# Kernel optimization log

Hardware: AMD Instinct MI355X
Metric: run time of the kernel (lower is better)

Reference implementation:

```python
import jax, jax.numpy as jnp
import numpy as np

B, S, H = 16, 512, 2048
NH, NKV = 16, 4
HD = H // NH  # 128


def _rope_tables(seq_len, dim, dtype):
    inv_freq = 1.0 / (10000.0 ** (jnp.arange(0, dim, 2, dtype=jnp.float32) / dim))
    t = jnp.arange(seq_len, dtype=jnp.float32)
    freqs = jnp.einsum('i,j->ij', t, inv_freq)          # [S, HD/2]
    emb = jnp.concatenate([freqs, freqs], axis=-1)       # [S, HD]
    cos = jnp.cos(emb)[None, None].astype(dtype)         # [1,1,S,HD]
    sin = jnp.sin(emb)[None, None].astype(dtype)
    return cos, sin


def _rotate_half(x):
    x1, x2 = jnp.split(x, 2, axis=-1)
    return jnp.concatenate([-x2, x1], axis=-1)


def setup_inputs() -> dict:
    key = jax.random.key(0)
    kx, kq, kk, kv, ko = jax.random.split(key, 5)
    x = jax.random.normal(kx, (B, S, H), dtype=jnp.float32)
    s = 0.02
    Wq = jax.random.normal(kq, (H, H), dtype=jnp.float32) * s
    Wk = jax.random.normal(kk, (NKV * HD, H), dtype=jnp.float32) * s
    Wv = jax.random.normal(kv, (NKV * HD, H), dtype=jnp.float32) * s
    Wo = jax.random.normal(ko, (H, H), dtype=jnp.float32) * s
    return {"x": x, "Wq": Wq, "Wk": Wk, "Wv": Wv, "Wo": Wo}


def reference(x, Wq, Wk, Wv, Wo):
    b, s, _ = x.shape
    scaling = HD ** -0.5
    # projections (torch Linear: y = x @ W.T, W is [out,in])
    q = jnp.einsum('bsh,oh->bso', x, Wq).reshape(b, s, NH, HD).transpose(0, 2, 1, 3)
    k = jnp.einsum('bsh,oh->bso', x, Wk).reshape(b, s, NKV, HD).transpose(0, 2, 1, 3)
    v = jnp.einsum('bsh,oh->bso', x, Wv).reshape(b, s, NKV, HD).transpose(0, 2, 1, 3)
    cos, sin = _rope_tables(s, HD, x.dtype)
    q = q * cos + _rotate_half(q) * sin
    k = k * cos + _rotate_half(k) * sin
    rep = NH // NKV
    k = jnp.repeat(k, rep, axis=1)  # [b, NH, s, HD]
    v = jnp.repeat(v, rep, axis=1)
    scores = jnp.einsum('bhqd,bhkd->bhqk', q, k) * scaling
    attn = jax.nn.softmax(scores, axis=-1)
    out = jnp.einsum('bhqk,bhkd->bhqd', attn, v)
    out = out.transpose(0, 2, 1, 3).reshape(b, s, H)
    return jnp.einsum('bsh,oh->bso', out, Wo)
```

## Files before the change

### kernel.cpp

```cpp
#include <hip/hip_runtime.h>
#include <stdint.h>


typedef _Float16 f16;
typedef _Float16 f16x4 __attribute__((ext_vector_type(4)));
typedef _Float16 f16x8 __attribute__((ext_vector_type(8)));
typedef float f32x4 __attribute__((ext_vector_type(4)));

#define B_   16
#define S_   512
#define H_   2048
#define NH_  16
#define NKV_ 4
#define HD_  128
#define ATT_SCALE 0.08838834764831843f
#define LOG2_10000_DIV64 0.20762050593045952f

#define AS1 __attribute__((address_space(1)))
#define AS3 __attribute__((address_space(3)))

__device__ __forceinline__ void async16(const void* g, const void* l) {
  __builtin_amdgcn_global_load_lds((const AS1 unsigned int*)(uintptr_t)g,
                                   (AS3 unsigned int*)(uintptr_t)l, 16, 0, 0);
}

__global__ __launch_bounds__(256) void cast_all(const float* __restrict__ x,
                                                const float* __restrict__ wq,
                                                const float* __restrict__ wk,
                                                const float* __restrict__ wv,
                                                const float* __restrict__ wo,
                                                f16* __restrict__ x_h,
                                                f16* __restrict__ w_h,
                                                f16* __restrict__ wo_h) {
  const int i = blockIdx.x * 256 + threadIdx.x;
  const float4* src;
  f16x4* dst;
  if (i < 4194304) {
    src = (const float4*)x + i;            dst = (f16x4*)x_h + i;
  } else if (i < 5242880) {
    int j = i - 4194304;
    src = (const float4*)wq + j;           dst = (f16x4*)w_h + j;
  } else if (i < 5505024) {
    int j = i - 5242880;
    src = (const float4*)wk + j;           dst = (f16x4*)w_h + 1048576 + j;
  } else if (i < 5767168) {
    int j = i - 5505024;
    src = (const float4*)wv + j;           dst = (f16x4*)w_h + 1310720 + j;
  } else {
    int j = i - 5767168;
    src = (const float4*)wo + j;           dst = (f16x4*)wo_h + j;
  }
  float4 v = *src;
  f16x4 o = {(f16)v.x, (f16)v.y, (f16)v.z, (f16)v.w};
  *dst = o;
}

template<int MODE>
__global__ __launch_bounds__(512, 2) void gemm_k(const f16* __restrict__ A,
                                                 const f16* __restrict__ W,
                                                 f16* __restrict__ qo,
                                                 f16* __restrict__ ko,
                                                 f16* __restrict__ vto,
                                                 float* __restrict__ fout) {
  __shared__ __align__(16) f16 As[3][256 * 64];
  __shared__ __align__(16) f16 Bs[3][128 * 64];
  const int K = 2048;
  const int NT = 32;
  const int m0 = blockIdx.x * 256;
  const int n0 = blockIdx.y * 128;
  const int tid = threadIdx.x;
  const int wave = tid >> 6, lane = tid & 63;
  const int quad = lane >> 4, l15 = lane & 15;
  const int wm = wave >> 1, wn = wave & 1;

  const f16* aptr[4];
  const f16* bptr[2];
#pragma unroll
  for (int i = 0; i < 4; ++i) {
    const int L = i * 512 + wave * 64 + lane;
    const int r = L >> 3, s = L & 7;
    aptr[i] = A + (size_t)(m0 + r) * K + (s ^ (r & 7)) * 8;
  }
#pragma unroll
  for (int i = 0; i < 2; ++i) {
    const int L = i * 512 + wave * 64 + lane;
    const int r = L >> 3, s = L & 7;
    bptr[i] = W + (size_t)(n0 + r) * K + (s ^ (r & 7)) * 8;
  }
  const int ldsw = wave * 1024;

  f32x4 acc[4][4] = {};
  f16x8 aC[4], bC[4], aN[4], bN[4];

  auto ldA = [&](f16x8* d, const f16* base, int ks) {
#pragma unroll
    for (int mi = 0; mi < 4; ++mi) {
      const int row = wm * 64 + mi * 16 + l15;
      const int slot = (ks * 4 + quad) ^ (l15 & 7);
      d[mi] = *reinterpret_cast<const f16x8*>(base + row * 64 + slot * 8);
    }
  };
  auto ldB = [&](f16x8* d, const f16* base, int ks) {
#pragma unroll
    for (int ni = 0; ni < 4; ++ni) {
      const int col = wn * 32 + (ni >> 1) * 64 + (ni & 1) * 16 + l15;
      const int slot = (ks * 4 + quad) ^ (l15 & 7);
      d[ni] = *reinterpret_cast<const f16x8*>(base + col * 64 + slot * 8);
    }
  };
  auto mfma16 = [&](const f16x8* Af, const f16x8* Bf) {
#pragma unroll
    for (int mi = 0; mi < 4; ++mi)
#pragma unroll
      for (int ni = 0; ni < 4; ++ni)
        acc[mi][ni] = __builtin_amdgcn_mfma_f32_16x16x32_f16(Af[mi], Bf[ni], acc[mi][ni], 0, 0, 0);
  };

#pragma unroll
  for (int t = 0; t < 2; ++t) {
#pragma unroll
    for (int i = 0; i < 4; ++i)
      async16(aptr[i] + t * 64, (const char*)&As[t][0] + i * 8192 + ldsw);
#pragma unroll
    for (int i = 0; i < 2; ++i)
      async16(bptr[i] + t * 64, (const char*)&Bs[t][0] + i * 8192 + ldsw);
  }
  asm volatile("s_waitcnt vmcnt(6)" ::: "memory");
  __builtin_amdgcn_s_barrier();
  ldA(aC, &As[0][0], 0);
  ldB(bC, &Bs[0][0], 0);

  for (int t = 0; t < NT; ++t) {
    const int buf = t % 3, bufn = (t + 1) % 3, bufs = (t + 2) % 3;
    const int sk = (t + 2) * 64;

    ldA(aN, &As[buf][0], 1);
    ldB(bN, &Bs[buf][0], 1);
    if (t + 2 < NT) {
      async16(aptr[0] + sk, (const char*)&As[bufs][0] + 0 * 8192 + ldsw);
      async16(aptr[1] + sk, (const char*)&As[bufs][0] + 1 * 8192 + ldsw);
      async16(bptr[0] + sk, (const char*)&Bs[bufs][0] + 0 * 8192 + ldsw);
    }
    asm volatile("s_waitcnt lgkmcnt(8)" ::: "memory");
    __builtin_amdgcn_sched_barrier(0);
    __builtin_amdgcn_s_setprio(1);
    mfma16(aC, bC);
    __builtin_amdgcn_s_setprio(0);

    if (t + 1 < NT) {
      if (t + 2 < NT) asm volatile("s_waitcnt vmcnt(3)" ::: "memory");
      else            asm volatile("s_waitcnt vmcnt(0)" ::: "memory");
      __builtin_amdgcn_s_barrier();
    }

    if (t + 1 < NT) {
      ldA(aC, &As[bufn][0], 0);
      ldB(bC, &Bs[bufn][0], 0);
    }
    if (t + 2 < NT) {
      async16(aptr[2] + sk, (const char*)&As[bufs][0] + 2 * 8192 + ldsw);
      async16(aptr[3] + sk, (const char*)&As[bufs][0] + 3 * 8192 + ldsw);
      async16(bptr[1] + sk, (const char*)&Bs[bufs][0] + 1 * 8192 + ldsw);
    }
    if (t + 1 < NT) asm volatile("s_waitcnt lgkmcnt(8)" ::: "memory");
    else            asm volatile("s_waitcnt lgkmcnt(0)" ::: "memory");
    __builtin_amdgcn_sched_barrier(0);
    __builtin_amdgcn_s_setprio(1);
    mfma16(aN, bN);
    __builtin_amdgcn_s_setprio(0);
    if (t + 1 < NT) __builtin_amdgcn_s_barrier();
  }

  if constexpr (MODE == 1) {
    const int b_ = m0 >> 9;
    if (n0 >= 2560) {
      const int h = (n0 - 2560) >> 7;
      f16* vb = vto + ((size_t)b_ * NKV_ + h) * HD_ * S_;
#pragma unroll
      for (int mi = 0; mi < 4; ++mi)
#pragma unroll
        for (int r = 0; r < 4; ++r) {
          const int s = (m0 + wm * 64 + mi * 16 + quad * 4 + r) & 511;
#pragma unroll
          for (int ni = 0; ni < 4; ++ni) {
            const int d = (ni >> 1) * 64 + wn * 32 + (ni & 1) * 16 + l15;
            vb[(size_t)d * S_ + s] = (f16)acc[mi][ni][r];
          }
        }
    } else {
      f16* ob = (n0 < 2048)
          ? (qo + ((size_t)b_ * NH_ + (n0 >> 7)) * S_ * HD_)
          : (ko + ((size_t)b_ * NKV_ + ((n0 - 2048) >> 7)) * S_ * HD_);
      float invf[2];
#pragma unroll
      for (int ni = 0; ni < 2; ++ni)
        invf[ni] = exp2f((float)(wn * 32 + ni * 16 + l15) * -LOG2_10000_DIV64);
#pragma unroll
      for (int mi = 0; mi < 4; ++mi)
#pragma unroll
        for (int r = 0; r < 4; ++r) {
          const int s = (m0 + wm * 64 + mi * 16 + quad * 4 + r) & 511;
          const size_t rb = (size_t)s * HD_;
#pragma unroll
          for (int ni = 0; ni < 2; ++ni) {
            const int d = wn * 32 + ni * 16 + l15;
            float sn, cs;
            __sincosf((float)s * invf[ni], &sn, &cs);
            const float x1 = acc[mi][ni][r], x2 = acc[mi][ni + 2][r];
            ob[rb + d] = (f16)(x1 * cs - x2 * sn);
            ob[rb + d + 64] = (f16)(x2 * cs + x1 * sn);
          }
        }
    }
  } else {
#pragma unroll
    for (int mi = 0; mi < 4; ++mi)
#pragma unroll
      for (int ni = 0; ni < 4; ++ni) {
        const int ncol = n0 + wn * 32 + (ni >> 1) * 64 + (ni & 1) * 16 + l15;
#pragma unroll
        for (int r = 0; r < 4; ++r) {
          const int mrow = m0 + wm * 64 + mi * 16 + quad * 4 + r;
          fout[(size_t)mrow * 2048 + ncol] = acc[mi][ni][r];
        }
      }
  }
}

__global__ __launch_bounds__(512) void attn_kernel(const f16* __restrict__ q,
                                                   const f16* __restrict__ k,
                                                   const f16* __restrict__ vt,
                                                   f16* __restrict__ out) {
  __shared__ __align__(16) f16 Kb[2][64 * 128];
  __shared__ __align__(16) f16 Vb[128 * 64];
  __shared__ __align__(16) f16 Ps[8][32 * 64];

  const int qt = blockIdx.x, h = blockIdx.y, b = blockIdx.z;
  const int kvh = h >> 2;
  const int tid = threadIdx.x;
  const int wave = tid >> 6, lane = tid & 63;
  const int quad = lane >> 4, l15 = lane & 15;

  const f16* qbase = q + (((size_t)b * NH_ + h) * S_ + qt * 256) * HD_;
  const f16* kbase = k + ((size_t)b * NKV_ + kvh) * S_ * HD_;
  const f16* vbase = vt + ((size_t)b * NKV_ + kvh) * HD_ * S_;

  auto stageK = [&](int j) {
    f16* dst = &Kb[j & 1][0];
#pragma unroll
    for (int i = 0; i < 2; ++i) {
      const int L0 = i * 512 + wave * 64;
      const int L = L0 + lane;
      const int r = L >> 4, c = L & 15;
      async16(kbase + (size_t)(j * 64 + r) * HD_ + (c ^ (r & 15)) * 8,
              (const char*)dst + (size_t)L0 * 16);
    }
  };
  auto stageV = [&](int j) {
#pragma unroll
    for (int i = 0; i < 2; ++i) {
      const int L0 = i * 512 + wave * 64;
      const int L = L0 + lane;
      const int r = L >> 3, c = L & 7;
      async16(vbase + (size_t)r * S_ + j * 64 + (c ^ (r & 7)) * 8,
              (const char*)&Vb[0] + (size_t)L0 * 16);
    }
  };

  f16x8 aq[2][4];
#pragma unroll
  for (int mi = 0; mi < 2; ++mi)
#pragma unroll
    for (int ks = 0; ks < 4; ++ks)
      aq[mi][ks] = *reinterpret_cast<const f16x8*>(
          qbase + (size_t)(wave * 32 + mi * 16 + l15) * HD_ + ks * 32 + quad * 8);

  stageK(0);

  f32x4 O[2][8] = {};
  float mrun[2][4], lrun[2][4];
#pragma unroll
  for (int mi = 0; mi < 2; ++mi)
#pragma unroll
    for (int r = 0; r < 4; ++r) { mrun[mi][r] = -3.0e38f; lrun[mi][r] = 0.f; }

  for (int j = 0; j < 8; ++j) {
    asm volatile("s_waitcnt vmcnt(0)" ::: "memory");
    __builtin_amdgcn_s_barrier();
    stageV(j);

    f32x4 Sc[2][4] = {};
#pragma unroll
    for (int ks = 0; ks < 4; ++ks) {
      f16x8 bk[4];
#pragma unroll
      for (int ni = 0; ni < 4; ++ni) {
        const int row = ni * 16 + l15;
        bk[ni] = *reinterpret_cast<const f16x8*>(
            &Kb[j & 1][row * 128 + (((ks * 4 + quad) ^ l15) & 15) * 8]);
      }
#pragma unroll
      for (int mi = 0; mi < 2; ++mi)
#pragma unroll
        for (int ni = 0; ni < 4; ++ni)
          Sc[mi][ni] = __builtin_amdgcn_mfma_f32_16x16x32_f16(aq[mi][ks], bk[ni], Sc[mi][ni], 0, 0, 0);
    }

#pragma unroll
    for (int mi = 0; mi < 2; ++mi)
#pragma unroll
      for (int r = 0; r < 4; ++r) {
        float mx = fmaxf(fmaxf(Sc[mi][0][r], Sc[mi][1][r]),
                         fmaxf(Sc[mi][2][r], Sc[mi][3][r]));
        mx *= ATT_SCALE;
#pragma unroll
        for (int off = 1; off < 16; off <<= 1) mx = fmaxf(mx, __shfl_xor(mx, off));
        const float mnew = fmaxf(mrun[mi][r], mx);
        const float alpha = __expf(mrun[mi][r] - mnew);
        float rs = 0.f;
#pragma unroll
        for (int ni = 0; ni < 4; ++ni) {
          const float pv = __expf(Sc[mi][ni][r] * ATT_SCALE - mnew);
          Sc[mi][ni][r] = pv;
          rs += pv;
        }
#pragma unroll
        for (int off = 1; off < 16; off <<= 1) rs += __shfl_xor(rs, off);
        lrun[mi][r] = lrun[mi][r] * alpha + rs;
        mrun[mi][r] = mnew;
#pragma unroll
        for (int ni = 0; ni < 8; ++ni) O[mi][ni][r] *= alpha;
        const int rowl = mi * 16 + quad * 4 + r;
#pragma unroll
        for (int ni = 0; ni < 4; ++ni) {
          const int col = ni * 16 + l15;
          Ps[wave][rowl * 64 + (((ni * 2 + (l15 >> 3)) ^ (rowl & 7)) << 3) + (l15 & 7)] =
              (f16)Sc[mi][ni][r];
        }
      }

    asm volatile("s_waitcnt vmcnt(0)" ::: "memory");
    __builtin_amdgcn_s_barrier();
    if (j < 7) stageK(j + 1);

#pragma unroll
    for (int ks = 0; ks < 2; ++ks) {
      f16x8 ap[2];
#pragma unroll
      for (int mi = 0; mi < 2; ++mi) {
        const int rowl = mi * 16 + l15;
        ap[mi] = *reinterpret_cast<const f16x8*>(
            &Ps[wave][rowl * 64 + (((ks * 4 + quad) ^ (l15 & 7)) << 3)]);
      }
#pragma unroll
      for (int ni = 0; ni < 8; ++ni) {
        const int row = ni * 16 + l15;
        const f16x8 bv = *reinterpret_cast<const f16x8*>(
            &Vb[row * 64 + (((ks * 4 + quad) ^ (l15 & 7)) << 3)]);
#pragma unroll
        for (int mi = 0; mi < 2; ++mi)
          O[mi][ni] = __builtin_amdgcn_mfma_f32_16x16x32_f16(ap[mi], bv, O[mi][ni], 0, 0, 0);
      }
    }
  }

#pragma unroll
  for (int mi = 0; mi < 2; ++mi)
#pragma unroll
    for (int r = 0; r < 4; ++r) {
      const float inv = 1.f / lrun[mi][r];
      const int srow = qt * 256 + wave * 32 + mi * 16 + quad * 4 + r;
#pragma unroll
      for (int ni = 0; ni < 8; ++ni)
        out[((size_t)b * S_ + srow) * H_ + h * HD_ + ni * 16 + l15] = (f16)(O[mi][ni][r] * inv);
    }
}

extern "C" void kernel_launch(void* const* d_in, const int* in_sizes, int n_in,
                              void* d_out, int out_size, void* d_ws, size_t ws_size,
                              hipStream_t stream) {
  const float* x = (const float*)d_in[0];
  const float* Wq = (const float*)d_in[1];
  const float* Wk = (const float*)d_in[2];
  const float* Wv = (const float*)d_in[3];
  const float* Wo = (const float*)d_in[4];
  float* out = (float*)d_out;
  char* ws = (char*)d_ws;

  f16* x_h  = (f16*)(ws + 0);
  f16* w_h  = (f16*)(ws + 33554432);
  f16* wo_h = (f16*)(ws + 46137344);
  f16* qb   = (f16*)(ws + 54525952);
  f16* kb   = (f16*)(ws + 88080384);
  f16* vtb  = (f16*)(ws + 96468992);
  f16* attn = (f16*)(ws + 104857600);

  cast_all<<<26624, 256, 0, stream>>>(x, Wq, Wk, Wv, Wo, x_h, w_h, wo_h);
  gemm_k<1><<<dim3(32, 24), 512, 0, stream>>>(x_h, w_h, qb, kb, vtb, nullptr);
  attn_kernel<<<dim3(2, 16, 16), 512, 0, stream>>>(qb, kb, vtb, attn);
  gemm_k<0><<<dim3(32, 16), 512, 0, stream>>>(attn, wo_h, nullptr, nullptr, nullptr, out);
}
```

Measured before the change: 385.6 us.

## Shrink GEMM K-tile to 32 with single-stage fragment pipeline

Halves the GEMM K-tile from 64 to 32, which doubles the number of main-loop iterations and halves the shared-memory footprint. The swizzle pattern is redone for the narrower tile, and the two-half fragment double-buffering is replaced by one fragment set per iteration, followed by a full lgkmcnt(0) wait. The launch bound's min-blocks hint is dropped. The intent is a simpler schedule and possibly higher occupancy, but fewer MFMAs per barrier and less overlap between LDS reads and MFMAs could expose latency.

```diff
diff --git a/kernel.cpp b/kernel.cpp
--- a/kernel.cpp
+++ b/kernel.cpp
@@ -56,16 +56,16 @@
 }
 
 template<int MODE>
-__global__ __launch_bounds__(512, 2) void gemm_k(const f16* __restrict__ A,
-                                                 const f16* __restrict__ W,
-                                                 f16* __restrict__ qo,
-                                                 f16* __restrict__ ko,
-                                                 f16* __restrict__ vto,
-                                                 float* __restrict__ fout) {
-  __shared__ __align__(16) f16 As[3][256 * 64];
-  __shared__ __align__(16) f16 Bs[3][128 * 64];
+__global__ __launch_bounds__(512) void gemm_s(const f16* __restrict__ A,
+                                              const f16* __restrict__ W,
+                                              f16* __restrict__ qo,
+                                              f16* __restrict__ ko,
+                                              f16* __restrict__ vto,
+                                              float* __restrict__ fout) {
+  __shared__ __align__(16) f16 As[3][256 * 32];
+  __shared__ __align__(16) f16 Bs[3][128 * 32];
   const int K = 2048;
-  const int NT = 32;
+  const int NT = 64;
   const int m0 = blockIdx.x * 256;
   const int n0 = blockIdx.y * 128;
   const int tid = threadIdx.x;
@@ -73,102 +73,74 @@
   const int quad = lane >> 4, l15 = lane & 15;
   const int wm = wave >> 1, wn = wave & 1;
 
-  const f16* aptr[4];
-  const f16* bptr[2];
-#pragma unroll
-  for (int i = 0; i < 4; ++i) {
-    const int L = i * 512 + wave * 64 + lane;
-    const int r = L >> 3, s = L & 7;
-    aptr[i] = A + (size_t)(m0 + r) * K + (s ^ (r & 7)) * 8;
-  }
-#pragma unroll
-  for (int i = 0; i < 2; ++i) {
-    const int L = i * 512 + wave * 64 + lane;
-    const int r = L >> 3, s = L & 7;
-    bptr[i] = W + (size_t)(n0 + r) * K + (s ^ (r & 7)) * 8;
+  const f16* aptr0;
+  const f16* aptr1;
+  const f16* bptr;
+  {
+    const int r0 = tid >> 2, c0 = tid & 3;
+    aptr0 = A + (size_t)(m0 + r0) * K + (c0 ^ ((r0 >> 1) & 3)) * 8;
+    const int G1 = tid + 512;
+    const int r1 = G1 >> 2, c1 = G1 & 3;
+    aptr1 = A + (size_t)(m0 + r1) * K + (c1 ^ ((r1 >> 1) & 3)) * 8;
+    const int rb = tid >> 2, cb = tid & 3;
+    bptr = W + (size_t)(n0 + rb) * K + (cb ^ ((rb >> 1) & 3)) * 8;
   }
   const int ldsw = wave * 1024;
 
+  int aoff[4], boff[4];
+#pragma unroll
+  for (int mi = 0; mi < 4; ++mi) {
+    const int row = wm * 64 + mi * 16 + l15;
+    aoff[mi] = row * 64 + (quad ^ ((row >> 1) & 3)) * 16;
+  }
+#pragma unroll
+  for (int ni = 0; ni < 4; ++ni) {
+    const int col = wn * 32 + (ni >> 1) * 64 + (ni & 1) * 16 + l15;
+    boff[ni] = col * 64 + (quad ^ ((col >> 1) & 3)) * 16;
+  }
+
   f32x4 acc[4][4] = {};
-  f16x8 aC[4], bC[4], aN[4], bN[4];
-
-  auto ldA = [&](f16x8* d, const f16* base, int ks) {
-#pragma unroll
-    for (int mi = 0; mi < 4; ++mi) {
-      const int row = wm * 64 + mi * 16 + l15;
-      const int slot = (ks * 4 + quad) ^ (l15 & 7);
-      d[mi] = *reinterpret_cast<const f16x8*>(base + row * 64 + slot * 8);
-    }
+  f16x8 af[4], bf[4];
+
+  auto STAGE = [&](int t, int buf) {
+    async16(aptr0 + t * 32, (const char*)&As[buf][0] + ldsw);
+    async16(aptr1 + t * 32, (const char*)&As[buf][0] + 8192 + ldsw);
+    async16(bptr + t * 32, (const char*)&Bs[buf][0] + ldsw);
   };
-  auto ldB = [&](f16x8* d, const f16* base, int ks) {
-#pragma unroll
-    for (int ni = 0; ni < 4; ++ni) {
-      const int col = wn * 32 + (ni >> 1) * 64 + (ni & 1) * 16 + l15;
-      const int slot = (ks * 4 + quad) ^ (l15 & 7);
-      d[ni] = *reinterpret_cast<const f16x8*>(base + col * 64 + slot * 8);
-    }
+  auto LDFRAGS = [&](int buf) {
+    const char* Ab = (const char*)&As[buf][0];
+    const char* Bb = (const char*)&Bs[buf][0];
+#pragma unroll
+    for (int mi = 0; mi < 4; ++mi)
+      af[mi] = *reinterpret_cast<const f16x8*>(Ab + aoff[mi]);
+#pragma unroll
+    for (int ni = 0; ni < 4; ++ni)
+      bf[ni] = *reinterpret_cast<const f16x8*>(Bb + boff[ni]);
   };
-  auto mfma16 = [&](const f16x8* Af, const f16x8* Bf) {
-#pragma unroll
-    for (int mi = 0; mi < 4; ++mi)
-#pragma unroll
-      for (int ni = 0; ni < 4; ++ni)
-        acc[mi][ni] = __builtin_amdgcn_mfma_f32_16x16x32_f16(Af[mi], Bf[ni], acc[mi][ni], 0, 0, 0);
-  };
-
-#pragma unroll
-  for (int t = 0; t < 2; ++t) {
-#pragma unroll
-    for (int i = 0; i < 4; ++i)
-      async16(aptr[i] + t * 64, (const char*)&As[t][0] + i * 8192 + ldsw);
-#pragma unroll
-    for (int i = 0; i < 2; ++i)
-      async16(bptr[i] + t * 64, (const char*)&Bs[t][0] + i * 8192 + ldsw);
-  }
-  asm volatile("s_waitcnt vmcnt(6)" ::: "memory");
+
+  STAGE(0, 0);
+  STAGE(1, 1);
+  asm volatile("s_waitcnt vmcnt(3)" ::: "memory");
   __builtin_amdgcn_s_barrier();
-  ldA(aC, &As[0][0], 0);
-  ldB(bC, &Bs[0][0], 0);
+  LDFRAGS(0);
 
   for (int t = 0; t < NT; ++t) {
-    const int buf = t % 3, bufn = (t + 1) % 3, bufs = (t + 2) % 3;
-    const int sk = (t + 2) * 64;
-
-    ldA(aN, &As[buf][0], 1);
-    ldB(bN, &Bs[buf][0], 1);
-    if (t + 2 < NT) {
-      async16(aptr[0] + sk, (const char*)&As[bufs][0] + 0 * 8192 + ldsw);
-      async16(aptr[1] + sk, (const char*)&As[bufs][0] + 1 * 8192 + ldsw);
-      async16(bptr[0] + sk, (const char*)&Bs[bufs][0] + 0 * 8192 + ldsw);
-    }
-    asm volatile("s_waitcnt lgkmcnt(8)" ::: "memory");
+    if (t + 2 < NT) STAGE(t + 2, (t + 2) % 3);
+    asm volatile("s_waitcnt lgkmcnt(0)" ::: "memory");
     __builtin_amdgcn_sched_barrier(0);
     __builtin_amdgcn_s_setprio(1);
-    mfma16(aC, bC);
+#pragma unroll
+    for (int mi = 0; mi < 4; ++mi)
+#pragma unroll
+      for (int ni = 0; ni < 4; ++ni)
+        acc[mi][ni] = __builtin_amdgcn_mfma_f32_16x16x32_f16(af[mi], bf[ni], acc[mi][ni], 0, 0, 0);
     __builtin_amdgcn_s_setprio(0);
-
     if (t + 1 < NT) {
       if (t + 2 < NT) asm volatile("s_waitcnt vmcnt(3)" ::: "memory");
       else            asm volatile("s_waitcnt vmcnt(0)" ::: "memory");
       __builtin_amdgcn_s_barrier();
-    }
-
-    if (t + 1 < NT) {
-      ldA(aC, &As[bufn][0], 0);
-      ldB(bC, &Bs[bufn][0], 0);
-    }
-    if (t + 2 < NT) {
-      async16(aptr[2] + sk, (const char*)&As[bufs][0] + 2 * 8192 + ldsw);
-      async16(aptr[3] + sk, (const char*)&As[bufs][0] + 3 * 8192 + ldsw);
-      async16(bptr[1] + sk, (const char*)&Bs[bufs][0] + 1 * 8192 + ldsw);
-    }
-    if (t + 1 < NT) asm volatile("s_waitcnt lgkmcnt(8)" ::: "memory");
-    else            asm volatile("s_waitcnt lgkmcnt(0)" ::: "memory");
-    __builtin_amdgcn_sched_barrier(0);
-    __builtin_amdgcn_s_setprio(1);
-    mfma16(aN, bN);
-    __builtin_amdgcn_s_setprio(0);
-    if (t + 1 < NT) __builtin_amdgcn_s_barrier();
+      LDFRAGS((t + 1) % 3);
+    }
   }
 
   if constexpr (MODE == 1) {
@@ -396,7 +368,7 @@
   f16* attn = (f16*)(ws + 104857600);
 
   cast_all<<<26624, 256, 0, stream>>>(x, Wq, Wk, Wv, Wo, x_h, w_h, wo_h);
-  gemm_k<1><<<dim3(32, 24), 512, 0, stream>>>(x_h, w_h, qb, kb, vtb, nullptr);
+  gemm_s<1><<<dim3(32, 24), 512, 0, stream>>>(x_h, w_h, qb, kb, vtb, nullptr);
   attn_kernel<<<dim3(2, 16, 16), 512, 0, stream>>>(qb, kb, vtb, attn);
-  gemm_k<0><<<dim3(32, 16), 512, 0, stream>>>(attn, wo_h, nullptr, nullptr, nullptr, out);
-}
+  gemm_s<0><<<dim3(32, 16), 512, 0, stream>>>(attn, wo_h, nullptr, nullptr, nullptr, out);
+}
```

Result: slower. 411.1 us (+6.6%).
